# Performance work log

Hardware: AMD Instinct MI355X
Metric: run time of the kernel (lower is better)

The kernel has to match this reference:

```python
import jax, jax.numpy as jnp
import numpy as np

OUT_F, IN_F, GROUP = 4096, 4096, 64  # meta['shape'] = (OUT_F, IN_F), group_size=64, axis=1
TOKENS = 8192  # batch*seq flattened


def dequant(W_q, scale, zero):
    # unpack_4bit_u8: high nibble = first half of rows, low nibble = second half
    hi = (W_q >> 4).astype(jnp.float32)
    lo = (W_q & 0xF).astype(jnp.float32)
    W_r = jnp.concatenate([hi, lo], axis=0)      # [G, GROUP]
    W_r = (W_r - zero) * scale                   # group-wise dequant (axis=1 grouping)
    return W_r.reshape(OUT_F, IN_F)


def setup_inputs() -> dict:
    key = jax.random.key(0)
    k0, k1, k2, k3, k4 = jax.random.split(key, 5)
    G = OUT_F * IN_F // GROUP  # 262144 groups
    x = jax.random.normal(k0, (TOKENS, IN_F), dtype=jnp.float32)
    W_q = jax.random.randint(k1, (G // 2, GROUP), 0, 256, dtype=jnp.int32)  # packed bytes
    scale = jax.random.uniform(k2, (G, 1), dtype=jnp.float32) * 0.01 + 1e-4  # 1/scale from quantizer
    zero = jax.random.uniform(k3, (G, 1), dtype=jnp.float32) * 15.0
    bias = jax.random.normal(k4, (OUT_F,), dtype=jnp.float32)
    return {"x": x, "W_q": W_q, "scale": scale, "zero": zero, "bias": bias}


def reference(x, W_q, scale, zero, bias):
    # HQQMatmulNoCacheDeq.forward: out = x @ dequantize().T + bias
    W_r = dequant(W_q, scale, zero)              # [OUT_F, IN_F]
    return x @ W_r.T + bias                      # [TOKENS, OUT_F]
```

## Files before the change

kernel.cpp:

```cpp
#include <hip/hip_runtime.h>
#include <stdint.h>


typedef __attribute__((ext_vector_type(8))) _Float16 half8;
typedef __attribute__((ext_vector_type(4))) float f32x4;

#define M_DIM 8192
#define N_DIM 4096
#define K_DIM 4096

__device__ __forceinline__ void async16(const void* g, void* l) {
  __builtin_amdgcn_global_load_lds(
      (const __attribute__((address_space(1))) void*)g,
      (__attribute__((address_space(3))) void*)l,
      16, 0, 0);
}

__global__ __launch_bounds__(256) void cvt_x_f16(const float* __restrict__ x,
                                                 _Float16* __restrict__ y) {
  const size_t i = ((size_t)blockIdx.x * 256 + threadIdx.x) * 8;
  f32x4 a = *(const f32x4*)(x + i);
  f32x4 b = *(const f32x4*)(x + i + 4);
  half8 h;
  h[0] = (_Float16)a[0]; h[1] = (_Float16)a[1];
  h[2] = (_Float16)a[2]; h[3] = (_Float16)a[3];
  h[4] = (_Float16)b[0]; h[5] = (_Float16)b[1];
  h[6] = (_Float16)b[2]; h[7] = (_Float16)b[3];
  *(half8*)(y + i) = h;
}

__global__ __launch_bounds__(256) void deq_w_f16(const int* __restrict__ Wq,
                                                 const float* __restrict__ scale,
                                                 const float* __restrict__ zero,
                                                 _Float16* __restrict__ W) {
  const int idx = blockIdx.x * 256 + threadIdx.x;
  const int o  = idx >> 9;
  const int kb = (idx & 511) << 3;
  const int g  = (o << 6) + (kb >> 6);
  const int j  = kb & 63;
  const bool hi = (o < 2048);
  const int* src = Wq + (size_t)(hi ? g : g - 131072) * 64 + j;
  const int4 v0 = *(const int4*)src;
  const int4 v1 = *(const int4*)(src + 4);
  const float s  = scale[g];
  const float nz = -zero[g] * s;
  int raw[8] = {v0.x, v0.y, v0.z, v0.w, v1.x, v1.y, v1.z, v1.w};
  half8 h;
#pragma unroll
  for (int r = 0; r < 8; ++r) {
    const int nib = hi ? ((raw[r] >> 4) & 0xF) : (raw[r] & 0xF);
    h[r] = (_Float16)((float)nib * s + nz);
  }
  *(half8*)(W + (size_t)o * K_DIM + kb) = h;
}

__global__ __launch_bounds__(256) void gemm_f16_ws(const _Float16* __restrict__ A,
                                                   const _Float16* __restrict__ B,
                                                   const float* __restrict__ bias,
                                                   float* __restrict__ C) {
  __shared__ _Float16 As[128 * 32];
  __shared__ _Float16 Bs[128 * 32];

  const int tid  = threadIdx.x;
  const int wave = tid >> 6;
  const int lane = tid & 63;
  const int quad = lane >> 4;
  const int l16  = lane & 15;

  const int m0 = blockIdx.y * 128;
  const int n0 = blockIdx.x * 128;
  const int wm = (wave & 1) * 64;
  const int wn = (wave >> 1) * 64;

  const int srow = tid >> 2;
  const int scol = (((tid & 3) ^ ((tid >> 3) & 3)) << 3);
  const _Float16* gA0 = A + (size_t)(m0 + srow) * K_DIM + scol;
  const _Float16* gA1 = gA0 + (size_t)64 * K_DIM;
  const _Float16* gB0 = B + (size_t)(n0 + srow) * K_DIM + scol;
  const _Float16* gB1 = gB0 + (size_t)64 * K_DIM;
  _Float16* ldsA = As + wave * 512;
  _Float16* ldsB = Bs + wave * 512;

  const int swz = (l16 >> 1) & 3;
  const int gA_off = ((quad ^ swz) << 3);

  f32x4 acc[4][4] = {};

  for (int k0 = 0; k0 < K_DIM; k0 += 32) {
    __syncthreads();
    async16(gA0 + k0, ldsA);
    async16(gA1 + k0, ldsA + 2048);
    async16(gB0 + k0, ldsB);
    async16(gB1 + k0, ldsB + 2048);
    __syncthreads();

    half8 aF[4], bF[4];
#pragma unroll
    for (int i = 0; i < 4; ++i)
      aF[i] = *(const half8*)(As + (wm + i * 16 + l16) * 32 + gA_off);
#pragma unroll
    for (int j = 0; j < 4; ++j)
      bF[j] = *(const half8*)(Bs + (wn + j * 16 + l16) * 32 + gA_off);
#pragma unroll
    for (int i = 0; i < 4; ++i)
#pragma unroll
      for (int j = 0; j < 4; ++j)
        acc[i][j] = __builtin_amdgcn_mfma_f32_16x16x32_f16(aF[i], bF[j],
                                                           acc[i][j], 0, 0, 0);
  }

#pragma unroll
  for (int j = 0; j < 4; ++j) {
    const int n = n0 + wn + j * 16 + l16;
    const float bv = bias[n];
#pragma unroll
    for (int i = 0; i < 4; ++i) {
      const int m = m0 + wm + i * 16 + quad * 4;
      float* p = C + (size_t)m * N_DIM + n;
      f32x4 v = acc[i][j];
      p[0 * N_DIM] = v[0] + bv;
      p[1 * N_DIM] = v[1] + bv;
      p[2 * N_DIM] = v[2] + bv;
      p[3 * N_DIM] = v[3] + bv;
    }
  }
}

__global__ __launch_bounds__(256) void gemm_fp32_fallback(
    const float* __restrict__ x, const int* __restrict__ Wq,
    const float* __restrict__ scale, const float* __restrict__ zero,
    const float* __restrict__ bias, float* __restrict__ C) {
  __shared__ float As[64][16];
  __shared__ float Bs[64][16];
  const int tid = threadIdx.x;
  const int m0 = blockIdx.y * 64;
  const int n0 = blockIdx.x * 64;
  const int tx = tid & 15;
  const int ty = tid >> 4;
  const int lr = tid >> 2;
  const int lc = (tid & 3) << 2;

  float acc[4][4] = {};

  for (int k0 = 0; k0 < K_DIM; k0 += 16) {
    __syncthreads();
    *(f32x4*)&As[lr][lc] = *(const f32x4*)(x + (size_t)(m0 + lr) * K_DIM + k0 + lc);
    {
      const int o = n0 + lr;
      const int k = k0 + lc;
      const int g = (o << 6) + (k >> 6);
      const bool hi = (o < 2048);
      const int* src = Wq + (size_t)(hi ? g : g - 131072) * 64 + (k & 63);
      const int4 v = *(const int4*)src;
      const float s = scale[g];
      const float nz = -zero[g] * s;
      f32x4 b;
      if (hi) {
        b[0] = (float)((v.x >> 4) & 0xF) * s + nz;
        b[1] = (float)((v.y >> 4) & 0xF) * s + nz;
        b[2] = (float)((v.z >> 4) & 0xF) * s + nz;
        b[3] = (float)((v.w >> 4) & 0xF) * s + nz;
      } else {
        b[0] = (float)(v.x & 0xF) * s + nz;
        b[1] = (float)(v.y & 0xF) * s + nz;
        b[2] = (float)(v.z & 0xF) * s + nz;
        b[3] = (float)(v.w & 0xF) * s + nz;
      }
      *(f32x4*)&Bs[lr][lc] = b;
    }
    __syncthreads();
#pragma unroll
    for (int kk = 0; kk < 16; ++kk) {
      float a[4], b[4];
#pragma unroll
      for (int r = 0; r < 4; ++r) a[r] = As[ty * 4 + r][kk];
#pragma unroll
      for (int c = 0; c < 4; ++c) b[c] = Bs[tx * 4 + c][kk];
#pragma unroll
      for (int r = 0; r < 4; ++r)
#pragma unroll
        for (int c = 0; c < 4; ++c) acc[r][c] += a[r] * b[c];
    }
  }
#pragma unroll
  for (int r = 0; r < 4; ++r)
#pragma unroll
    for (int c = 0; c < 4; ++c) {
      const int n = n0 + tx * 4 + c;
      C[(size_t)(m0 + ty * 4 + r) * N_DIM + n] = acc[r][c] + bias[n];
    }
}

extern "C" void kernel_launch(void* const* d_in, const int* in_sizes, int n_in,
                              void* d_out, int out_size, void* d_ws, size_t ws_size,
                              hipStream_t stream) {
  const float* x     = (const float*)d_in[0];
  const int*   Wq    = (const int*)d_in[1];
  const float* scale = (const float*)d_in[2];
  const float* zero  = (const float*)d_in[3];
  const float* bias  = (const float*)d_in[4];
  float* out = (float*)d_out;

  const size_t xh_bytes = (size_t)M_DIM * K_DIM * 2;
  const size_t wh_bytes = (size_t)N_DIM * K_DIM * 2;

  if (ws_size >= xh_bytes + wh_bytes) {
    _Float16* xh = (_Float16*)d_ws;
    _Float16* wh = (_Float16*)((char*)d_ws + xh_bytes);
    cvt_x_f16<<<M_DIM * K_DIM / (256 * 8), 256, 0, stream>>>(x, xh);
    deq_w_f16<<<N_DIM * K_DIM / (256 * 8), 256, 0, stream>>>(Wq, scale, zero, wh);
    dim3 grid(N_DIM / 128, M_DIM / 128);
    gemm_f16_ws<<<grid, 256, 0, stream>>>(xh, wh, bias, out);
  } else {
    dim3 grid(N_DIM / 64, M_DIM / 64);
    gemm_fp32_fallback<<<grid, 256, 0, stream>>>(x, Wq, scale, zero, bias, out);
  }
}
```

Before: 570.6 us.

## Merge prep kernels and use deep triple-buffered 256x256 GEMM tiles

Merges the x conversion and weight dequant into a single prep launch. Replaces the 128x128 GEMM with a 256x256 tile using 8 waves, triple-buffered async LDS loads with vmcnt-based waits, a block-index swizzle for L2 locality, and s_setprio around the MFMA bursts. This targets the load-sync stall of the old single-buffered loop, which waited on global loads every K step, and raises per-block reuse. In exchange it uses 96KB of LDS and 128 accumulator registers per thread, which may limit occupancy.

```diff
diff --git a/kernel.cpp b/kernel.cpp
--- a/kernel.cpp
+++ b/kernel.cpp
@@ -16,106 +16,151 @@
       16, 0, 0);
 }
 
-__global__ __launch_bounds__(256) void cvt_x_f16(const float* __restrict__ x,
-                                                 _Float16* __restrict__ y) {
-  const size_t i = ((size_t)blockIdx.x * 256 + threadIdx.x) * 8;
-  f32x4 a = *(const f32x4*)(x + i);
-  f32x4 b = *(const f32x4*)(x + i + 4);
-  half8 h;
-  h[0] = (_Float16)a[0]; h[1] = (_Float16)a[1];
-  h[2] = (_Float16)a[2]; h[3] = (_Float16)a[3];
-  h[4] = (_Float16)b[0]; h[5] = (_Float16)b[1];
-  h[6] = (_Float16)b[2]; h[7] = (_Float16)b[3];
-  *(half8*)(y + i) = h;
-}
-
-__global__ __launch_bounds__(256) void deq_w_f16(const int* __restrict__ Wq,
-                                                 const float* __restrict__ scale,
-                                                 const float* __restrict__ zero,
-                                                 _Float16* __restrict__ W) {
-  const int idx = blockIdx.x * 256 + threadIdx.x;
-  const int o  = idx >> 9;
-  const int kb = (idx & 511) << 3;
-  const int g  = (o << 6) + (kb >> 6);
-  const int j  = kb & 63;
-  const bool hi = (o < 2048);
-  const int* src = Wq + (size_t)(hi ? g : g - 131072) * 64 + j;
-  const int4 v0 = *(const int4*)src;
-  const int4 v1 = *(const int4*)(src + 4);
-  const float s  = scale[g];
-  const float nz = -zero[g] * s;
-  int raw[8] = {v0.x, v0.y, v0.z, v0.w, v1.x, v1.y, v1.z, v1.w};
-  half8 h;
-#pragma unroll
-  for (int r = 0; r < 8; ++r) {
-    const int nib = hi ? ((raw[r] >> 4) & 0xF) : (raw[r] & 0xF);
-    h[r] = (_Float16)((float)nib * s + nz);
-  }
-  *(half8*)(W + (size_t)o * K_DIM + kb) = h;
-}
-
-__global__ __launch_bounds__(256) void gemm_f16_ws(const _Float16* __restrict__ A,
-                                                   const _Float16* __restrict__ B,
-                                                   const float* __restrict__ bias,
-                                                   float* __restrict__ C) {
-  __shared__ _Float16 As[128 * 32];
-  __shared__ _Float16 Bs[128 * 32];
+__global__ __launch_bounds__(256) void prep(
+    const float* __restrict__ x, const int* __restrict__ Wq,
+    const float* __restrict__ scale, const float* __restrict__ zero,
+    _Float16* __restrict__ xh, _Float16* __restrict__ wh) {
+  const int b = blockIdx.x;
+  if (b < 16384) {
+    const size_t i = ((size_t)b * 256 + threadIdx.x) * 8;
+    f32x4 a = *(const f32x4*)(x + i);
+    f32x4 c = *(const f32x4*)(x + i + 4);
+    half8 h;
+    h[0] = (_Float16)a[0]; h[1] = (_Float16)a[1];
+    h[2] = (_Float16)a[2]; h[3] = (_Float16)a[3];
+    h[4] = (_Float16)c[0]; h[5] = (_Float16)c[1];
+    h[6] = (_Float16)c[2]; h[7] = (_Float16)c[3];
+    *(half8*)(xh + i) = h;
+  } else {
+    const int idx = (b - 16384) * 256 + threadIdx.x;
+    const int o  = idx >> 9;
+    const int kb = (idx & 511) << 3;
+    const int g  = (o << 6) + (kb >> 6);
+    const int j  = kb & 63;
+    const bool hi = (o < 2048);
+    const int* src = Wq + (size_t)(hi ? g : g - 131072) * 64 + j;
+    const int4 v0 = *(const int4*)src;
+    const int4 v1 = *(const int4*)(src + 4);
+    const float s  = scale[g];
+    const float nz = -zero[g] * s;
+    int raw[8] = {v0.x, v0.y, v0.z, v0.w, v1.x, v1.y, v1.z, v1.w};
+    half8 h;
+#pragma unroll
+    for (int r = 0; r < 8; ++r) {
+      const int nib = hi ? ((raw[r] >> 4) & 0xF) : (raw[r] & 0xF);
+      h[r] = (_Float16)((float)nib * s + nz);
+    }
+    *(half8*)(wh + (size_t)o * K_DIM + kb) = h;
+  }
+}
+
+__global__ __launch_bounds__(512, 2) void gemm_f16_deep(
+    const _Float16* __restrict__ A, const _Float16* __restrict__ B,
+    const float* __restrict__ bias, float* __restrict__ C) {
+  __shared__ _Float16 As[3 * 8192];
+  __shared__ _Float16 Bs[3 * 8192];
 
   const int tid  = threadIdx.x;
   const int wave = tid >> 6;
   const int lane = tid & 63;
   const int quad = lane >> 4;
   const int l16  = lane & 15;
-
-  const int m0 = blockIdx.y * 128;
-  const int n0 = blockIdx.x * 128;
-  const int wm = (wave & 1) * 64;
-  const int wn = (wave >> 1) * 64;
+  const int wm   = wave >> 2;
+  const int wn   = wave & 3;
+
+  const int bid = blockIdx.x;
+  const int swb = (bid & 7) * 64 + (bid >> 3);
+  const int m0 = (swb >> 4) * 256;
+  const int n0 = (swb & 15) * 256;
 
   const int srow = tid >> 2;
-  const int scol = (((tid & 3) ^ ((tid >> 3) & 3)) << 3);
-  const _Float16* gA0 = A + (size_t)(m0 + srow) * K_DIM + scol;
-  const _Float16* gA1 = gA0 + (size_t)64 * K_DIM;
-  const _Float16* gB0 = B + (size_t)(n0 + srow) * K_DIM + scol;
-  const _Float16* gB1 = gB0 + (size_t)64 * K_DIM;
-  _Float16* ldsA = As + wave * 512;
-  _Float16* ldsB = Bs + wave * 512;
-
-  const int swz = (l16 >> 1) & 3;
-  const int gA_off = ((quad ^ swz) << 3);
-
-  f32x4 acc[4][4] = {};
-
-  for (int k0 = 0; k0 < K_DIM; k0 += 32) {
-    __syncthreads();
-    async16(gA0 + k0, ldsA);
-    async16(gA1 + k0, ldsA + 2048);
-    async16(gB0 + k0, ldsB);
-    async16(gB1 + k0, ldsB + 2048);
-    __syncthreads();
-
+  const int sg   = (((tid & 3) ^ ((srow >> 1) & 3)) << 3);
+  const _Float16* gA0 = A + (size_t)(m0 + srow) * K_DIM + sg;
+  const _Float16* gA1 = gA0 + (size_t)128 * K_DIM;
+  const _Float16* gB0 = B + (size_t)(n0 + srow) * K_DIM + sg;
+  const _Float16* gB1 = gB0 + (size_t)128 * K_DIM;
+  const int wst = wave * 512;
+
+  const int fro  = ((quad ^ ((l16 >> 1) & 3)) << 3);
+  const int arow = wm * 128 + l16;
+  const int brow = wn * 64 + l16;
+
+  f32x4 acc[8][4] = {};
+
+  int sR = 0, sN = 8192, sW = 16384;
+
+  async16(gA0,      As + sR + wst);
+  async16(gA1,      As + sR + 4096 + wst);
+  async16(gB0,      Bs + sR + wst);
+  async16(gB1,      Bs + sR + 4096 + wst);
+  async16(gA0 + 32, As + sN + wst);
+  async16(gA1 + 32, As + sN + 4096 + wst);
+  async16(gB0 + 32, Bs + sN + wst);
+  async16(gB1 + 32, Bs + sN + 4096 + wst);
+  asm volatile("s_waitcnt vmcnt(4)" ::: "memory");
+  __builtin_amdgcn_s_barrier();
+
+  const int NT = K_DIM / 32;
+#pragma unroll 1
+  for (int T = 0; T < NT; ++T) {
+    if (T + 2 < NT) {
+      const int kk = (T + 2) * 32;
+      async16(gA0 + kk, As + sW + wst);
+      async16(gA1 + kk, As + sW + 4096 + wst);
+      async16(gB0 + kk, Bs + sW + wst);
+      async16(gB1 + kk, Bs + sW + 4096 + wst);
+    }
+
+    const _Float16* Ab = As + sR;
+    const _Float16* Bb = Bs + sR;
     half8 aF[4], bF[4];
 #pragma unroll
-    for (int i = 0; i < 4; ++i)
-      aF[i] = *(const half8*)(As + (wm + i * 16 + l16) * 32 + gA_off);
-#pragma unroll
     for (int j = 0; j < 4; ++j)
-      bF[j] = *(const half8*)(Bs + (wn + j * 16 + l16) * 32 + gA_off);
+      bF[j] = *(const half8*)(Bb + (brow + j * 16) * 32 + fro);
+#pragma unroll
+    for (int i = 0; i < 4; ++i)
+      aF[i] = *(const half8*)(Ab + (arow + i * 16) * 32 + fro);
+
+    __builtin_amdgcn_s_setprio(1);
 #pragma unroll
     for (int i = 0; i < 4; ++i)
 #pragma unroll
       for (int j = 0; j < 4; ++j)
         acc[i][j] = __builtin_amdgcn_mfma_f32_16x16x32_f16(aF[i], bF[j],
                                                            acc[i][j], 0, 0, 0);
+    __builtin_amdgcn_s_setprio(0);
+
+#pragma unroll
+    for (int i = 0; i < 4; ++i)
+      aF[i] = *(const half8*)(Ab + (arow + 64 + i * 16) * 32 + fro);
+
+    __builtin_amdgcn_s_setprio(1);
+#pragma unroll
+    for (int i = 0; i < 4; ++i)
+#pragma unroll
+      for (int j = 0; j < 4; ++j)
+        acc[i + 4][j] = __builtin_amdgcn_mfma_f32_16x16x32_f16(aF[i], bF[j],
+                                                               acc[i + 4][j],
+                                                               0, 0, 0);
+    __builtin_amdgcn_s_setprio(0);
+
+    if (T + 2 < NT) {
+      asm volatile("s_waitcnt vmcnt(4)" ::: "memory");
+      __builtin_amdgcn_s_barrier();
+    } else if (T + 1 < NT) {
+      asm volatile("s_waitcnt vmcnt(0)" ::: "memory");
+      __builtin_amdgcn_s_barrier();
+    }
+    const int t = sR; sR = sN; sN = sW; sW = t;
   }
 
 #pragma unroll
   for (int j = 0; j < 4; ++j) {
-    const int n = n0 + wn + j * 16 + l16;
+    const int n = n0 + wn * 64 + j * 16 + l16;
     const float bv = bias[n];
 #pragma unroll
-    for (int i = 0; i < 4; ++i) {
-      const int m = m0 + wm + i * 16 + quad * 4;
+    for (int i = 0; i < 8; ++i) {
+      const int m = m0 + wm * 128 + i * 16 + quad * 4;
       float* p = C + (size_t)m * N_DIM + n;
       f32x4 v = acc[i][j];
       p[0 * N_DIM] = v[0] + bv;
@@ -207,10 +252,8 @@
   if (ws_size >= xh_bytes + wh_bytes) {
     _Float16* xh = (_Float16*)d_ws;
     _Float16* wh = (_Float16*)((char*)d_ws + xh_bytes);
-    cvt_x_f16<<<M_DIM * K_DIM / (256 * 8), 256, 0, stream>>>(x, xh);
-    deq_w_f16<<<N_DIM * K_DIM / (256 * 8), 256, 0, stream>>>(Wq, scale, zero, wh);
-    dim3 grid(N_DIM / 128, M_DIM / 128);
-    gemm_f16_ws<<<grid, 256, 0, stream>>>(xh, wh, bias, out);
+    prep<<<16384 + 8192, 256, 0, stream>>>(x, Wq, scale, zero, xh, wh);
+    gemm_f16_deep<<<(M_DIM / 256) * (N_DIM / 256), 512, 0, stream>>>(xh, wh, bias, out);
   } else {
     dim3 grid(N_DIM / 64, M_DIM / 64);
     gemm_fp32_fallback<<<grid, 256, 0, stream>>>(x, Wq, scale, zero, bias, out);
```

Result: slower. 591.0 us (+3.6%).
